# Kernel optimization log

Measured on AMD Instinct MI355X. Metric: run time of the kernel, lower is better.

Reference implementation:

```python
import jax, jax.numpy as jnp
import numpy as np

B, T, D = 2, 1024, 2048
H, HKV, DH = 16, 4, 128
G = H // HKV  # GQA groups
F = 5632
ROPE_THETA = 10000.0
EPS = 1e-6


def _rope_tables(t, dh, theta):
    inv = 1.0 / (theta ** (np.arange(0, dh, 2, dtype=np.float32) / dh))  # [dh//2]
    ang = np.outer(np.arange(t, dtype=np.float32), inv)                  # [T, dh//2]
    return jnp.asarray(np.cos(ang)), jnp.asarray(np.sin(ang))


def setup_inputs() -> dict:
    key = jax.random.key(0)
    ks = jax.random.split(key, 9)
    s = 0.02
    cos, sin = _rope_tables(T, DH, ROPE_THETA)
    return {
        "x": jax.random.normal(ks[0], (B, T, D), jnp.float32),
        "freqs_cos": cos,
        "freqs_sin": sin,
        "w_norm1": jnp.ones((D,), jnp.float32),
        "w_norm2": jnp.ones((D,), jnp.float32),
        "wq": jax.random.normal(ks[1], (D, H * DH), jnp.float32) * s,
        "wk": jax.random.normal(ks[2], (D, HKV * DH), jnp.float32) * s,
        "wv": jax.random.normal(ks[3], (D, HKV * DH), jnp.float32) * s,
        "wo": jax.random.normal(ks[4], (D, D), jnp.float32) * s,
        "w1": jax.random.normal(ks[5], (D, F), jnp.float32) * s,
        "w2": jax.random.normal(ks[6], (F, D), jnp.float32) * s,
        "w3": jax.random.normal(ks[7], (D, F), jnp.float32) * s,
    }


def _rmsnorm(x, w):
    var = jnp.mean(jnp.square(x), axis=-1, keepdims=True)
    return x * jax.lax.rsqrt(var + EPS) * w


def _apply_rope(x, cos, sin):
    # x: [B, T, nH, DH]; cos/sin: [T, DH//2]
    xr = x.reshape(*x.shape[:-1], DH // 2, 2)
    x0, x1 = xr[..., 0], xr[..., 1]
    c = cos[None, :, None, :]
    s = sin[None, :, None, :]
    o0 = x0 * c - x1 * s
    o1 = x0 * s + x1 * c
    return jnp.stack([o0, o1], axis=-1).reshape(x.shape)


def reference(x, freqs_cos, freqs_sin, w_norm1, w_norm2, wq, wk, wv, wo, w1, w2, w3):
    residual = x
    xn = _rmsnorm(x, w_norm1)
    q = (xn @ wq).reshape(B, T, H, DH)
    k = (xn @ wk).reshape(B, T, HKV, DH)
    v = (xn @ wv).reshape(B, T, HKV, DH)
    q = _apply_rope(q, freqs_cos, freqs_sin)
    k = _apply_rope(k, freqs_cos, freqs_sin)
    # grouped heads: q -> [B, HKV, G, T, DH]; k,v -> [B, HKV, T, DH]
    q = q.transpose(0, 2, 1, 3).reshape(B, HKV, G, T, DH)
    k = k.transpose(0, 2, 1, 3)
    v = v.transpose(0, 2, 1, 3)
    scale = DH ** -0.5
    scores = jnp.einsum("bkgtd,bksd->bkgts", q, k) * scale  # [B,HKV,G,T,T]
    causal = jnp.tril(jnp.ones((T, T), dtype=bool))
    scores = jnp.where(causal, scores, -jnp.inf)
    attn = jax.nn.softmax(scores, axis=-1)
    out = jnp.einsum("bkgts,bksd->bkgtd", attn, v)  # [B,HKV,G,T,DH]
    out = out.reshape(B, H, T, DH).transpose(0, 2, 1, 3).reshape(B, T, D)
    x = residual + out @ wo
    h = _rmsnorm(x, w_norm2)
    ffn = (jax.nn.silu(h @ w1) * (h @ w3)) @ w2
    return x + ffn
```

## Files before the change

### kernel.cpp

```cpp
#include <hip/hip_runtime.h>
#include <hip/hip_bf16.h>
#include <math.h>

typedef __hip_bfloat16 bf16;
typedef __attribute__((ext_vector_type(8))) short bf16x8;
typedef __attribute__((ext_vector_type(4))) float f32x4;

__device__ __forceinline__ float b2f(bf16 v) { return __bfloat162float(v); }
__device__ __forceinline__ bf16  f2b(float v) { return __float2bfloat16(v); }

constexpr int Bc = 2, Tc = 1024, Dc = 2048, Hc = 16, HKVc = 4, DHc = 128, Fc = 5632;
constexpr int Mr = Bc * Tc;
constexpr int Nqkv = Hc * DHc + 2 * HKVc * DHc;

__device__ __forceinline__ void g2l16(void* lds, const void* g) {
  __builtin_amdgcn_global_load_lds(
      (const __attribute__((address_space(1))) unsigned int*)g,
      (__attribute__((address_space(3))) unsigned int*)lds, 16, 0, 0);
}

__global__ __launch_bounds__(256) void tcast_k(const float* __restrict__ src,
                                               bf16* __restrict__ dst,
                                               int N, int K) {
  __shared__ bf16 tile[64][68];
  const int t = threadIdx.x;
  const int n0 = blockIdx.x * 64, k0 = blockIdx.y * 64;
#pragma unroll
  for (int it = 0; it < 4; ++it) {
    const int kl = it * 16 + (t >> 4);
    const int nl = (t & 15) * 4;
    float4 v = *reinterpret_cast<const float4*>(src + (size_t)(k0 + kl) * N + n0 + nl);
    tile[kl][nl]     = f2b(v.x);
    tile[kl][nl + 1] = f2b(v.y);
    tile[kl][nl + 2] = f2b(v.z);
    tile[kl][nl + 3] = f2b(v.w);
  }
  __syncthreads();
  union { uint4 u; bf16 h[8]; } o;
#pragma unroll
  for (int it = 0; it < 2; ++it) {
    const int nl = it * 32 + (t >> 3);
    const int kl = (t & 7) * 8;
#pragma unroll
    for (int j = 0; j < 8; ++j) o.h[j] = tile[kl + j][nl];
    *reinterpret_cast<uint4*>(dst + (size_t)(n0 + nl) * K + k0 + kl) = o.u;
  }
}

__global__ __launch_bounds__(256) void tcast_ffn(const float* __restrict__ src,
                                                 bf16* __restrict__ dst,
                                                 int off) {
  __shared__ bf16 tile[64][68];
  const int t = threadIdx.x;
  const int n0 = blockIdx.x * 64, k0 = blockIdx.y * 64;
#pragma unroll
  for (int it = 0; it < 4; ++it) {
    const int kl = it * 16 + (t >> 4);
    const int nl = (t & 15) * 4;
    float4 v = *reinterpret_cast<const float4*>(src + (size_t)(k0 + kl) * Fc + n0 + nl);
    tile[kl][nl]     = f2b(v.x);
    tile[kl][nl + 1] = f2b(v.y);
    tile[kl][nl + 2] = f2b(v.z);
    tile[kl][nl + 3] = f2b(v.w);
  }
  __syncthreads();
  union { uint4 u; bf16 h[8]; } o;
#pragma unroll
  for (int it = 0; it < 2; ++it) {
    const int nl = it * 32 + (t >> 3);
    const int kl = (t & 7) * 8;
#pragma unroll
    for (int j = 0; j < 8; ++j) o.h[j] = tile[kl + j][nl];
    const int n = n0 + nl;
    const int r = ((n >> 4) << 5) + (n & 15) + off;
    *reinterpret_cast<uint4*>(dst + (size_t)r * Dc + k0 + kl) = o.u;
  }
}

__global__ __launch_bounds__(256) void rmsnorm_k(const float* __restrict__ x,
                                                 const float* __restrict__ w,
                                                 bf16* __restrict__ out) {
  const size_t rbase = (size_t)blockIdx.x * Dc;
  float ss = 0.f;
  for (int i = threadIdx.x; i < Dc; i += 256) {
    float v = x[rbase + i];
    ss += v * v;
  }
#pragma unroll
  for (int off = 32; off > 0; off >>= 1) ss += __shfl_down(ss, off, 64);
  __shared__ float red[4];
  const int lane = threadIdx.x & 63, wid = threadIdx.x >> 6;
  if (lane == 0) red[wid] = ss;
  __syncthreads();
  const float scale = rsqrtf((red[0] + red[1] + red[2] + red[3]) / (float)Dc + 1e-6f);
  for (int i = threadIdx.x; i < Dc; i += 256)
    out[rbase + i] = f2b(x[rbase + i] * scale * w[i]);
}

__global__ __launch_bounds__(256) void reduce4_rms(const float* __restrict__ P,
                                                   const float* __restrict__ x,
                                                   const float* __restrict__ w,
                                                   float* __restrict__ xat,
                                                   bf16* __restrict__ hb) {
  constexpr size_t PS = (size_t)Mr * Dc;
  const size_t base4 = (size_t)blockIdx.x * (Dc / 4);
  const int t = threadIdx.x;
  float4 v[2];
  float ss = 0.f;
#pragma unroll
  for (int j = 0; j < 2; ++j) {
    const size_t c4 = base4 + t + j * 256;
    float4 a = reinterpret_cast<const float4*>(x)[c4];
#pragma unroll
    for (int z = 0; z < 4; ++z) {
      float4 q = reinterpret_cast<const float4*>(P + z * PS)[c4];
      a.x += q.x; a.y += q.y; a.z += q.z; a.w += q.w;
    }
    reinterpret_cast<float4*>(xat)[c4] = a;
    ss += a.x * a.x + a.y * a.y + a.z * a.z + a.w * a.w;
    v[j] = a;
  }
#pragma unroll
  for (int off = 32; off > 0; off >>= 1) ss += __shfl_down(ss, off, 64);
  __shared__ float red[4];
  const int lane = t & 63, wid = t >> 6;
  if (lane == 0) red[wid] = ss;
  __syncthreads();
  const float scale = rsqrtf((red[0] + red[1] + red[2] + red[3]) / (float)Dc + 1e-6f);
  bf16* hrow = hb + (size_t)blockIdx.x * Dc;
#pragma unroll
  for (int j = 0; j < 2; ++j) {
    const int c = (t + j * 256) * 4;
    hrow[c]     = f2b(v[j].x * scale * w[c]);
    hrow[c + 1] = f2b(v[j].y * scale * w[c + 1]);
    hrow[c + 2] = f2b(v[j].z * scale * w[c + 2]);
    hrow[c + 3] = f2b(v[j].w * scale * w[c + 3]);
  }
}

__global__ __launch_bounds__(256) void reduce4_add(const float* __restrict__ P,
                                                   const float* __restrict__ res,
                                                   float* __restrict__ out) {
  constexpr size_t PS = (size_t)Mr * Dc;
  const size_t c4 = (size_t)blockIdx.x * 256 + threadIdx.x;
  float4 a = reinterpret_cast<const float4*>(res)[c4];
#pragma unroll
  for (int z = 0; z < 4; ++z) {
    float4 q = reinterpret_cast<const float4*>(P + z * PS)[c4];
    a.x += q.x; a.y += q.y; a.z += q.z; a.w += q.w;
  }
  reinterpret_cast<float4*>(out)[c4] = a;
}

template <int K>
__global__ __launch_bounds__(512, 2) void ffn_gemm256(const bf16* __restrict__ A,
                                                      const bf16* __restrict__ B,
                                                      bf16* __restrict__ act) {
  constexpr int NT = K / 64;
  constexpr int NIT = NT / 2;
  __shared__ bf16 As[2 * 256 * 64];
  __shared__ bf16 Bs[3 * 256 * 64];
  const int tid = threadIdx.x;
  const int lane = tid & 63, wv = tid >> 6;
  const int wr = wv >> 2, wc = wv & 3;
  const int fr = lane & 15, quad = lane >> 4;
  const int swz = fr & 7;
  const int bm = blockIdx.y * 256;
  const int bn = blockIdx.x * 256;
  const int lrow = tid >> 3;
  const int scol = ((tid & 7) ^ (lrow & 7)) * 8;
  const size_t rstep = (size_t)64 * K;

  auto stageA = [&](int t, int half) {
    const int buf = (t & 1) * 16384;
    const bf16* g = A + (size_t)(bm + half * 128 + lrow) * K + t * 64 + scol;
    bf16* d = As + buf + half * 8192 + (size_t)tid * 8;
    g2l16(d, g);
    g2l16(d + 4096, g + rstep);
  };
  auto stageB = [&](int t, int half, int buf) {
    const bf16* g = B + (size_t)(bn + half * 128 + lrow) * K + t * 64 + scol;
    bf16* d = Bs + buf * 16384 + half * 8192 + (size_t)tid * 8;
    g2l16(d, g);
    g2l16(d + 4096, g + rstep);
  };

  f32x4 acc[8][4] = {};
  const int u0 = (quad ^ swz) * 8;

  stageA(0, 0); stageA(0, 1);
  stageB(0, 0, 0); stageB(0, 1, 0);
  stageB(1, 0, 1); stageB(1, 1, 1);
  asm volatile("s_waitcnt vmcnt(4)" ::: "memory");
  __builtin_amdgcn_s_barrier();

  int rb0 = 0, rb1 = 1, sb = 2;
  for (int it = 0; it < NIT; ++it) {
    const int t1 = 2 * it + 1;
#pragma unroll
    for (int j = 0; j < 8; ++j) {
      const int bufT = (j < 4) ? 0 : 16384;
      const int bufB = ((j < 4) ? rb0 : rb1) * 16384;
      const int qr4 = ((j & 3) >> 1) * 4, qc2 = ((j & 3) & 1) * 2;
      bf16x8 af[4][2], bv[2][2];
      const bf16* Ab = As + bufT + (size_t)(wr * 128 + fr) * 64;
      const bf16* Bb = Bs + bufB + (size_t)(wc * 64 + fr) * 64;
#pragma unroll
      for (int ii = 0; ii < 4; ++ii) {
        af[ii][0] = *reinterpret_cast<const bf16x8*>(Ab + (qr4 + ii) * 1024 + u0);
        af[ii][1] = *reinterpret_cast<const bf16x8*>(Ab + (qr4 + ii) * 1024 + (u0 ^ 32));
      }
#pragma unroll
      for (int jj = 0; jj < 2; ++jj) {
        bv[jj][0] = *reinterpret_cast<const bf16x8*>(Bb + (qc2 + jj) * 1024 + u0);
        bv[jj][1] = *reinterpret_cast<const bf16x8*>(Bb + (qc2 + jj) * 1024 + (u0 ^ 32));
      }
      if (j == 0)      stageA(t1, 0);
      else if (j == 1) stageA(t1, 1);
      else if (j == 2) { if (2 * it + 2 < NT) stageB(2 * it + 2, 0, sb); }
      else if (j == 3) { if (2 * it + 2 < NT) stageB(2 * it + 2, 1, sb); }
      else if (j == 4) { if (2 * it + 2 < NT) stageA(2 * it + 2, 0); }
      else if (j == 5) { if (2 * it + 2 < NT) stageA(2 * it + 2, 1); }
      else if (j == 6) { if (2 * it + 3 < NT) stageB(2 * it + 3, 0, rb0); }
      else             { if (2 * it + 3 < NT) stageB(2 * it + 3, 1, rb0); }
      __builtin_amdgcn_s_barrier();
      asm volatile("s_waitcnt lgkmcnt(0)" ::: "memory");
      __builtin_amdgcn_sched_barrier(0);
      __builtin_amdgcn_s_setprio(1);
#pragma unroll
      for (int ii = 0; ii < 4; ++ii)
#pragma unroll
        for (int jj = 0; jj < 2; ++jj) {
          acc[qr4 + ii][qc2 + jj] = __builtin_amdgcn_mfma_f32_16x16x32_bf16(
              af[ii][0], bv[jj][0], acc[qr4 + ii][qc2 + jj], 0, 0, 0);
          acc[qr4 + ii][qc2 + jj] = __builtin_amdgcn_mfma_f32_16x16x32_bf16(
              af[ii][1], bv[jj][1], acc[qr4 + ii][qc2 + jj], 0, 0, 0);
        }
      __builtin_amdgcn_s_setprio(0);
      if (j == 3) {
        if (2 * it + 2 < NT) asm volatile("s_waitcnt vmcnt(4)" ::: "memory");
        else                 asm volatile("s_waitcnt vmcnt(0)" ::: "memory");
      } else if (j == 7) {
        if (2 * it + 3 < NT)      asm volatile("s_waitcnt vmcnt(4)" ::: "memory");
        else if (2 * it + 2 < NT) asm volatile("s_waitcnt vmcnt(0)" ::: "memory");
      }
      __builtin_amdgcn_s_barrier();
    }
    const int nrb0 = sb; sb = rb1; rb1 = rb0; rb0 = nrb0;
  }

  const int er = quad * 4, ec = lane & 15;
#pragma unroll
  for (int i = 0; i < 8; ++i) {
    const int row = bm + wr * 128 + i * 16 + er;
#pragma unroll
    for (int jp = 0; jp < 2; ++jp) {
      const f32x4 g = acc[i][2 * jp], u = acc[i][2 * jp + 1];
      const int f = blockIdx.x * 128 + wc * 32 + jp * 16 + ec;
#pragma unroll
      for (int r = 0; r < 4; ++r) {
        const float sg = g[r] / (1.f + __expf(-g[r]));
        act[(size_t)(row + r) * Fc + f] = f2b(sg * u[r]);
      }
    }
  }
}

template <int KFULL, int KSUB>
__global__ __launch_bounds__(512, 2) void gemm256sk(const bf16* __restrict__ A,
                                                    const bf16* __restrict__ Bt,
                                                    float* __restrict__ Part,
                                                    int N) {
  constexpr int NT = KSUB / 64;
  constexpr int NIT = NT / 2;
  __shared__ bf16 As[2 * 256 * 64];
  __shared__ bf16 Bs[3 * 256 * 64];
  const int tid = threadIdx.x;
  const int lane = tid & 63, wv = tid >> 6;
  const int wr = wv >> 2, wc = wv & 3;
  const int fr = lane & 15, quad = lane >> 4;
  const int swz = fr & 7;
  const int bm = blockIdx.y * 256;
  const int bn = blockIdx.x * 256;
  const int kbase = blockIdx.z * KSUB;
  const int lrow = tid >> 3;
  const int scol = ((tid & 7) ^ (lrow & 7)) * 8;
  const size_t rstep = (size_t)64 * KFULL;

  auto stageA = [&](int t, int half) {
    const int buf = (t & 1) * 16384;
    const bf16* g = A + (size_t)(bm + half * 128 + lrow) * KFULL + kbase + t * 64 + scol;
    bf16* d = As + buf + half * 8192 + (size_t)tid * 8;
    g2l16(d, g);
    g2l16(d + 4096, g + rstep);
  };
  auto stageB = [&](int t, int half, int buf) {
    const bf16* g = Bt + (size_t)(bn + half * 128 + lrow) * KFULL + kbase + t * 64 + scol;
    bf16* d = Bs + buf * 16384 + half * 8192 + (size_t)tid * 8;
    g2l16(d, g);
    g2l16(d + 4096, g + rstep);
  };

  f32x4 acc[8][4] = {};
  const int u0 = (quad ^ swz) * 8;

  stageA(0, 0); stageA(0, 1);
  stageB(0, 0, 0); stageB(0, 1, 0);
  stageB(1, 0, 1); stageB(1, 1, 1);
  asm volatile("s_waitcnt vmcnt(4)" ::: "memory");
  __builtin_amdgcn_s_barrier();

  int rb0 = 0, rb1 = 1, sb = 2;
  for (int it = 0; it < NIT; ++it) {
    const int t1 = 2 * it + 1;
#pragma unroll
    for (int j = 0; j < 8; ++j) {
      const int bufT = (j < 4) ? 0 : 16384;
      const int bufB = ((j < 4) ? rb0 : rb1) * 16384;
      const int qr4 = ((j & 3) >> 1) * 4, qc2 = ((j & 3) & 1) * 2;
      bf16x8 af[4][2], bv[2][2];
      const bf16* Ab = As + bufT + (size_t)(wr * 128 + fr) * 64;
      const bf16* Bb = Bs + bufB + (size_t)(wc * 64 + fr) * 64;
#pragma unroll
      for (int ii = 0; ii < 4; ++ii) {
        af[ii][0] = *reinterpret_cast<const bf16x8*>(Ab + (qr4 + ii) * 1024 + u0);
        af[ii][1] = *reinterpret_cast<const bf16x8*>(Ab + (qr4 + ii) * 1024 + (u0 ^ 32));
      }
#pragma unroll
      for (int jj = 0; jj < 2; ++jj) {
        bv[jj][0] = *reinterpret_cast<const bf16x8*>(Bb + (qc2 + jj) * 1024 + u0);
        bv[jj][1] = *reinterpret_cast<const bf16x8*>(Bb + (qc2 + jj) * 1024 + (u0 ^ 32));
      }
      if (j == 0)      stageA(t1, 0);
      else if (j == 1) stageA(t1, 1);
      else if (j == 2) { if (2 * it + 2 < NT) stageB(2 * it + 2, 0, sb); }
      else if (j == 3) { if (2 * it + 2 < NT) stageB(2 * it + 2, 1, sb); }
      else if (j == 4) { if (2 * it + 2 < NT) stageA(2 * it + 2, 0); }
      else if (j == 5) { if (2 * it + 2 < NT) stageA(2 * it + 2, 1); }
      else if (j == 6) { if (2 * it + 3 < NT) stageB(2 * it + 3, 0, rb0); }
      else             { if (2 * it + 3 < NT) stageB(2 * it + 3, 1, rb0); }
      __builtin_amdgcn_s_barrier();
      asm volatile("s_waitcnt lgkmcnt(0)" ::: "memory");
      __builtin_amdgcn_sched_barrier(0);
      __builtin_amdgcn_s_setprio(1);
#pragma unroll
      for (int ii = 0; ii < 4; ++ii)
#pragma unroll
        for (int jj = 0; jj < 2; ++jj) {
          acc[qr4 + ii][qc2 + jj] = __builtin_amdgcn_mfma_f32_16x16x32_bf16(
              af[ii][0], bv[jj][0], acc[qr4 + ii][qc2 + jj], 0, 0, 0);
          acc[qr4 + ii][qc2 + jj] = __builtin_amdgcn_mfma_f32_16x16x32_bf16(
              af[ii][1], bv[jj][1], acc[qr4 + ii][qc2 + jj], 0, 0, 0);
        }
      __builtin_amdgcn_s_setprio(0);
      if (j == 3) {
        if (2 * it + 2 < NT) asm volatile("s_waitcnt vmcnt(4)" ::: "memory");
        else                 asm volatile("s_waitcnt vmcnt(0)" ::: "memory");
      } else if (j == 7) {
        if (2 * it + 3 < NT)      asm volatile("s_waitcnt vmcnt(4)" ::: "memory");
        else if (2 * it + 2 < NT) asm volatile("s_waitcnt vmcnt(0)" ::: "memory");
      }
      __builtin_amdgcn_s_barrier();
    }
    const int nrb0 = sb; sb = rb1; rb1 = rb0; rb0 = nrb0;
  }

  float* P = Part + (size_t)blockIdx.z * ((size_t)Mr * N);
  const int er = quad * 4, ec = lane & 15;
#pragma unroll
  for (int i = 0; i < 8; ++i) {
    const int row = bm + wr * 128 + i * 16 + er;
#pragma unroll
    for (int jc = 0; jc < 4; ++jc) {
      const int col = bn + wc * 64 + jc * 16 + ec;
#pragma unroll
      for (int r = 0; r < 4; ++r)
        P[(size_t)(row + r) * N + col] = acc[i][jc][r];
    }
  }
}

__global__ __launch_bounds__(256) void repack_k(const float* __restrict__ P,
                                                const float* __restrict__ cosb,
                                                const float* __restrict__ sinb,
                                                bf16* __restrict__ Qr,
                                                bf16* __restrict__ Kr,
                                                bf16* __restrict__ Vt) {
  constexpr size_t PS = (size_t)Mr * Nqkv;
  const int bt = blockIdx.x;
  const int b = bt >> 10, tp = bt & (Tc - 1);
  const int t0 = threadIdx.x;
  const float* r0 = P + (size_t)bt * Nqkv;
  const float* r1 = r0 + PS;
#pragma unroll
  for (int k = 0; k < 4; ++k) {
    int p2 = k * 256 + t0;
    int hh = p2 >> 6, i = p2 & 63;
    float c = cosb[tp * 64 + i], sn = sinb[tp * 64 + i];
    float2 v0 = *reinterpret_cast<const float2*>(r0 + hh * 128 + 2 * i);
    float2 v1 = *reinterpret_cast<const float2*>(r1 + hh * 128 + 2 * i);
    float x0 = v0.x + v1.x, x1 = v0.y + v1.y;
    bf16* dst = Qr + ((size_t)(b * Hc + hh) * Tc + tp) * DHc + 2 * i;
    dst[0] = f2b(x0 * c - x1 * sn);
    dst[1] = f2b(x0 * sn + x1 * c);
  }
  {
    int hh = t0 >> 6, i = t0 & 63;
    float c = cosb[tp * 64 + i], sn = sinb[tp * 64 + i];
    float2 v0 = *reinterpret_cast<const float2*>(r0 + 2048 + hh * 128 + 2 * i);
    float2 v1 = *reinterpret_cast<const float2*>(r1 + 2048 + hh * 128 + 2 * i);
    float x0 = v0.x + v1.x, x1 = v0.y + v1.y;
    bf16* dst = Kr + ((size_t)(b * HKVc + hh) * Tc + tp) * DHc + 2 * i;
    dst[0] = f2b(x0 * c - x1 * sn);
    dst[1] = f2b(x0 * sn + x1 * c);
  }
#pragma unroll
  for (int k = 0; k < 2; ++k) {
    int e = k * 256 + t0;
    int kvh = e >> 7, dd = e & 127;
    Vt[((size_t)(b * HKVc + kvh) * DHc + dd) * Tc + tp] = f2b(r0[2560 + e] + r1[2560 + e]);
  }
}

__global__ __launch_bounds__(256) void fattn(const bf16* __restrict__ Qr,
                                             const bf16* __restrict__ Kr,
                                             const bf16* __restrict__ Vt,
                                             bf16* __restrict__ ao) {
  __shared__ __align__(16) bf16 Ks[2][64 * 128];
  __shared__ __align__(16) bf16 Vts[2][128 * 64];
  __shared__ __align__(16) bf16 Ps[4][16 * 72];
  const int idx = blockIdx.x;
  const int r = idx & 15;
  const int qt = (r & 1) ? (15 - (r >> 1)) : (r >> 1);
  const int h = (idx >> 4) & 15;
  const int b = idx >> 8;
  const int kv = h >> 2;
  const int t = threadIdx.x, lane = t & 63, wv = t >> 6;
  const int fr = lane & 15, quad = lane >> 4;

  const bf16* Qbase = Qr + ((size_t)(b * Hc + h) * Tc + qt * 64) * DHc;
  const bf16* Kbase = Kr + (size_t)(b * HKVc + kv) * Tc * DHc;
  const bf16* Vbase = Vt + (size_t)(b * HKVc + kv) * DHc * Tc;

  auto stageK = [&](int kt, int buf) {
    const bf16* src = Kbase + (size_t)kt * 64 * DHc;
#pragma unroll
    for (int rr = 0; rr < 4; ++rr) {
      const int row = rr * 16 + (t >> 4);
      const int cS = (t & 15) ^ (row & 7);
      g2l16(&Ks[buf][rr * 2048 + t * 8], src + row * DHc + cS * 8);
    }
  };
  auto stageV = [&](int kt, int buf) {
#pragma unroll
    for (int rr = 0; rr < 4; ++rr) {
      const int row = rr * 32 + (t >> 3);
      const int cS = (t & 7) ^ (row & 7);
      g2l16(&Vts[buf][rr * 2048 + t * 8], Vbase + (size_t)row * Tc + kt * 64 + cS * 8);
    }
  };

  bf16x8 qf[4];
#pragma unroll
  for (int c = 0; c < 4; ++c)
    qf[c] = *reinterpret_cast<const bf16x8*>(Qbase + (size_t)(wv * 16 + fr) * DHc + c * 32 + quad * 8);

  float m[4], l[4];
  f32x4 o[8] = {};
#pragma unroll
  for (int r2 = 0; r2 < 4; ++r2) { m[r2] = -3.0e38f; l[r2] = 0.f; }

  stageK(0, 0);
  stageV(0, 0);
  __syncthreads();
  int buf = 0;

  for (int kt = 0; kt <= qt; ++kt) {
    if (kt < qt) { stageK(kt + 1, buf ^ 1); stageV(kt + 1, buf ^ 1); }
    const int sw = fr & 7;
    f32x4 s[4];
    __builtin_amdgcn_s_setprio(1);
#pragma unroll
    for (int cb = 0; cb < 4; ++cb) {
      f32x4 acc = {};
#pragma unroll
      for (int kc = 0; kc < 4; ++kc) {
        bf16x8 kf = *reinterpret_cast<const bf16x8*>(
            &Ks[buf][(cb * 16 + fr) * 128 + (((kc << 2) + quad) ^ sw) * 8]);
        acc = __builtin_amdgcn_mfma_f32_16x16x32_bf16(qf[kc], kf, acc, 0, 0, 0);
      }
      s[cb] = acc * 0.08838834764831845f;
    }
    __builtin_amdgcn_s_setprio(0);
    if (kt == qt) {
#pragma unroll
      for (int cb = 0; cb < 4; ++cb)
#pragma unroll
        for (int r2 = 0; r2 < 4; ++r2) {
          int key = cb * 16 + fr;
          int qg = wv * 16 + quad * 4 + r2;
          if (key > qg) s[cb][r2] = -3.0e38f;
        }
    }
    float tm[4], ts[4];
#pragma unroll
    for (int r2 = 0; r2 < 4; ++r2)
      tm[r2] = fmaxf(fmaxf(s[0][r2], s[1][r2]), fmaxf(s[2][r2], s[3][r2]));
#pragma unroll
    for (int off = 1; off < 16; off <<= 1)
#pragma unroll
      for (int r2 = 0; r2 < 4; ++r2)
        tm[r2] = fmaxf(tm[r2], __shfl_xor(tm[r2], off, 64));
    float al[4];
#pragma unroll
    for (int r2 = 0; r2 < 4; ++r2) {
      float mn = fmaxf(m[r2], tm[r2]);
      al[r2] = __expf(m[r2] - mn);
      m[r2] = mn;
      ts[r2] = 0.f;
    }
#pragma unroll
    for (int cb = 0; cb < 4; ++cb)
#pragma unroll
      for (int r2 = 0; r2 < 4; ++r2) {
        float e = __expf(s[cb][r2] - m[r2]);
        s[cb][r2] = e;
        ts[r2] += e;
      }
#pragma unroll
    for (int off = 1; off < 16; off <<= 1)
#pragma unroll
      for (int r2 = 0; r2 < 4; ++r2)
        ts[r2] += __shfl_xor(ts[r2], off, 64);
#pragma unroll
    for (int r2 = 0; r2 < 4; ++r2) l[r2] = l[r2] * al[r2] + ts[r2];
#pragma unroll
    for (int db = 0; db < 8; ++db)
#pragma unroll
      for (int r2 = 0; r2 < 4; ++r2) o[db][r2] *= al[r2];
    bf16* pw = Ps[wv];
#pragma unroll
    for (int cb = 0; cb < 4; ++cb)
#pragma unroll
      for (int r2 = 0; r2 < 4; ++r2)
        pw[(quad * 4 + r2) * 72 + cb * 16 + fr] = f2b(s[cb][r2]);
    bf16x8 pa[2];
    pa[0] = *reinterpret_cast<const bf16x8*>(&pw[fr * 72 + quad * 8]);
    pa[1] = *reinterpret_cast<const bf16x8*>(&pw[fr * 72 + 32 + quad * 8]);
    __builtin_amdgcn_s_setprio(1);
#pragma unroll
    for (int db = 0; db < 8; ++db) {
      bf16x8 v0 = *reinterpret_cast<const bf16x8*>(
          &Vts[buf][(db * 16 + fr) * 64 + (quad ^ sw) * 8]);
      bf16x8 v1 = *reinterpret_cast<const bf16x8*>(
          &Vts[buf][(db * 16 + fr) * 64 + ((4 + quad) ^ sw) * 8]);
      o[db] = __builtin_amdgcn_mfma_f32_16x16x32_bf16(pa[0], v0, o[db], 0, 0, 0);
      o[db] = __builtin_amdgcn_mfma_f32_16x16x32_bf16(pa[1], v1, o[db], 0, 0, 0);
    }
    __builtin_amdgcn_s_setprio(0);
    __syncthreads();
    buf ^= 1;
  }
#pragma unroll
  for (int r2 = 0; r2 < 4; ++r2) {
    float inv = 1.f / l[r2];
    int qg = qt * 64 + wv * 16 + quad * 4 + r2;
    bf16* orow = ao + (size_t)(b * Tc + qg) * Dc + h * DHc;
#pragma unroll
    for (int db = 0; db < 8; ++db)
      orow[db * 16 + fr] = f2b(o[db][r2] * inv);
  }
}

extern "C" void kernel_launch(void* const* d_in, const int* in_sizes, int n_in,
                              void* d_out, int out_size, void* d_ws, size_t ws_size,
                              hipStream_t stream) {
  const float* x    = (const float*)d_in[0];
  const float* fcos = (const float*)d_in[1];
  const float* fsin = (const float*)d_in[2];
  const float* wn1  = (const float*)d_in[3];
  const float* wn2  = (const float*)d_in[4];
  const float* wq   = (const float*)d_in[5];
  const float* wk   = (const float*)d_in[6];
  const float* wv   = (const float*)d_in[7];
  const float* wo   = (const float*)d_in[8];
  const float* w1   = (const float*)d_in[9];
  const float* w2   = (const float*)d_in[10];
  const float* w3   = (const float*)d_in[11];

  char* p = (char*)d_ws;
  bf16* wqkv_t = (bf16*)p;                 p += (size_t)Nqkv * Dc * 2;
  float* xat   = (float*)d_ws;
  bf16* wo_t = (bf16*)p;                   p += (size_t)Dc * Dc * 2;
  bf16* w13t = (bf16*)p;                   p += (size_t)2 * Fc * Dc * 2;
  bf16* w2t  = w13t;
  bf16* xn   = (bf16*)p;                   p += (size_t)Mr * Dc * 2;
  bf16* ao   = (bf16*)p;                   p += (size_t)Mr * Dc * 2;
  bf16* act  = (bf16*)p;                   p += (size_t)Mr * Fc * 2;
  float* Pbuf = (float*)p;                 p += (size_t)4 * Mr * Dc * 4;
  bf16* hb = xn;
  bf16* Qr = act;
  bf16* Kr = act + (size_t)Mr * Hc * DHc;
  bf16* Vtb = Kr + (size_t)Mr * HKVc * DHc;

  const dim3 blk(256);
  tcast_k<<<dim3(32, 32), blk, 0, stream>>>(wq, wqkv_t, 2048, 2048);
  tcast_k<<<dim3(8, 32), blk, 0, stream>>>(wk, wqkv_t + (size_t)2048 * 2048, 512, 2048);
  tcast_k<<<dim3(8, 32), blk, 0, stream>>>(wv, wqkv_t + (size_t)2560 * 2048, 512, 2048);
  tcast_k<<<dim3(32, 32), blk, 0, stream>>>(wo, wo_t, 2048, 2048);
  tcast_ffn<<<dim3(88, 32), blk, 0, stream>>>(w1, w13t, 0);
  tcast_ffn<<<dim3(88, 32), blk, 0, stream>>>(w3, w13t, 16);

  rmsnorm_k<<<Mr, blk, 0, stream>>>(x, wn1, xn);
  gemm256sk<Dc, 1024><<<dim3(Nqkv / 256, Mr / 256, 2), dim3(512), 0, stream>>>(xn, wqkv_t, Pbuf, Nqkv);
  repack_k<<<Mr, blk, 0, stream>>>(Pbuf, fcos, fsin, Qr, Kr, Vtb);
  fattn<<<Bc * Hc * 16, blk, 0, stream>>>(Qr, Kr, Vtb, ao);
  gemm256sk<Dc, 512><<<dim3(Dc / 256, Mr / 256, 4), dim3(512), 0, stream>>>(ao, wo_t, Pbuf, Dc);
  reduce4_rms<<<Mr, blk, 0, stream>>>(Pbuf, x, wn2, xat, hb);
  ffn_gemm256<Dc><<<dim3(2 * Fc / 256, Mr / 256), dim3(512), 0, stream>>>(hb, w13t, act);
  tcast_k<<<dim3(32, 88), blk, 0, stream>>>(w2, w2t, 2048, 5632);
  gemm256sk<Fc, 1408><<<dim3(Dc / 256, Mr / 256, 4), dim3(512), 0, stream>>>(act, w2t, Pbuf, Dc);
  reduce4_add<<<Mr * Dc / 1024, blk, 0, stream>>>(Pbuf, xat, (float*)d_out);
}
```

Measured before the change: 561.0 us.

## Fuse weight transposes into GEMM launches to overlap casts with compute

Merges the wq/wk/wv transpose-casts and the first rmsnorm into one launch. It also folds the wo/w1/w3 transpose-casts into the QKV GEMM grid and the w2 transpose-cast into the FFN gate/up GEMM grid, with extra blocks taking the bandwidth-bound cast work. The goal is to cut launch count and let memory-bound casting run alongside MFMA-bound GEMM tiles. The w2 cast gets its own workspace region when space allows, so it no longer has to wait for the w13 buffer to be freed. The cost is larger monolithic kernels with 160KB of LDS per block for the cast blocks, which may limit occupancy for the cast work.

Measured after the change: 529.7 us. 1.06x faster.

```diff
diff --git a/kernel.cpp b/kernel.cpp
--- a/kernel.cpp
+++ b/kernel.cpp
@@ -19,12 +19,10 @@
       (__attribute__((address_space(3))) unsigned int*)lds, 16, 0, 0);
 }
 
-__global__ __launch_bounds__(256) void tcast_k(const float* __restrict__ src,
-                                               bf16* __restrict__ dst,
-                                               int N, int K) {
-  __shared__ bf16 tile[64][68];
-  const int t = threadIdx.x;
-  const int n0 = blockIdx.x * 64, k0 = blockIdx.y * 64;
+__device__ __forceinline__ void tcast_tile(const float* __restrict__ src,
+                                           bf16* __restrict__ dst,
+                                           int N, int K, int n0, int k0,
+                                           int t, bf16 (*tile)[68]) {
 #pragma unroll
   for (int it = 0; it < 4; ++it) {
     const int kl = it * 16 + (t >> 4);
@@ -47,12 +45,10 @@
   }
 }
 
-__global__ __launch_bounds__(256) void tcast_ffn(const float* __restrict__ src,
-                                                 bf16* __restrict__ dst,
-                                                 int off) {
-  __shared__ bf16 tile[64][68];
-  const int t = threadIdx.x;
-  const int n0 = blockIdx.x * 64, k0 = blockIdx.y * 64;
+__device__ __forceinline__ void tcast_ffn_tile(const float* __restrict__ src,
+                                               bf16* __restrict__ dst, int off,
+                                               int n0, int k0, int t,
+                                               bf16 (*tile)[68]) {
 #pragma unroll
   for (int it = 0; it < 4; ++it) {
     const int kl = it * 16 + (t >> 4);
@@ -77,10 +73,11 @@
   }
 }
 
-__global__ __launch_bounds__(256) void rmsnorm_k(const float* __restrict__ x,
-                                                 const float* __restrict__ w,
-                                                 bf16* __restrict__ out) {
-  const size_t rbase = (size_t)blockIdx.x * Dc;
+__device__ __forceinline__ void rmsnorm_row(const float* __restrict__ x,
+                                            const float* __restrict__ w,
+                                            bf16* __restrict__ out,
+                                            int row, float* red) {
+  const size_t rbase = (size_t)row * Dc;
   float ss = 0.f;
   for (int i = threadIdx.x; i < Dc; i += 256) {
     float v = x[rbase + i];
@@ -88,13 +85,34 @@
   }
 #pragma unroll
   for (int off = 32; off > 0; off >>= 1) ss += __shfl_down(ss, off, 64);
-  __shared__ float red[4];
   const int lane = threadIdx.x & 63, wid = threadIdx.x >> 6;
   if (lane == 0) red[wid] = ss;
   __syncthreads();
   const float scale = rsqrtf((red[0] + red[1] + red[2] + red[3]) / (float)Dc + 1e-6f);
   for (int i = threadIdx.x; i < Dc; i += 256)
     out[rbase + i] = f2b(x[rbase + i] * scale * w[i]);
+}
+
+__global__ __launch_bounds__(256) void prep1(const float* __restrict__ wq,
+                                             const float* __restrict__ wk,
+                                             const float* __restrict__ wv,
+                                             const float* __restrict__ x,
+                                             const float* __restrict__ wn1,
+                                             bf16* __restrict__ wqkv_t,
+                                             bf16* __restrict__ xn) {
+  __shared__ __align__(16) bf16 tile[64][68];
+  const int b = blockIdx.x;
+  if (b < 1024) {
+    tcast_tile(wq, wqkv_t, 2048, 2048, (b & 31) * 64, (b >> 5) * 64, threadIdx.x, tile);
+  } else if (b < 1280) {
+    const int r = b - 1024;
+    tcast_tile(wk, wqkv_t + (size_t)2048 * 2048, 512, 2048, (r & 7) * 64, (r >> 3) * 64, threadIdx.x, tile);
+  } else if (b < 1536) {
+    const int r = b - 1280;
+    tcast_tile(wv, wqkv_t + (size_t)2560 * 2048, 512, 2048, (r & 7) * 64, (r >> 3) * 64, threadIdx.x, tile);
+  } else {
+    rmsnorm_row(x, wn1, xn, b - 1536, (float*)tile);
+  }
 }
 
 __global__ __launch_bounds__(256) void reduce4_rms(const float* __restrict__ P,
@@ -152,21 +170,174 @@
   reinterpret_cast<float4*>(out)[c4] = a;
 }
 
-template <int K>
-__global__ __launch_bounds__(512, 2) void ffn_gemm256(const bf16* __restrict__ A,
-                                                      const bf16* __restrict__ B,
-                                                      bf16* __restrict__ act) {
-  constexpr int NT = K / 64;
+template <int KFULL, int KSUB>
+__device__ __forceinline__ void gemm256sk_dev(const bf16* __restrict__ A,
+                                              const bf16* __restrict__ Bt,
+                                              float* __restrict__ Part,
+                                              int N, int bx, int by, int bz,
+                                              char* smem) {
+  constexpr int NT = KSUB / 64;
   constexpr int NIT = NT / 2;
-  __shared__ bf16 As[2 * 256 * 64];
-  __shared__ bf16 Bs[3 * 256 * 64];
+  bf16* As = (bf16*)smem;
+  bf16* Bs = (bf16*)(smem + 65536);
   const int tid = threadIdx.x;
   const int lane = tid & 63, wv = tid >> 6;
   const int wr = wv >> 2, wc = wv & 3;
   const int fr = lane & 15, quad = lane >> 4;
   const int swz = fr & 7;
-  const int bm = blockIdx.y * 256;
-  const int bn = blockIdx.x * 256;
+  const int bm = by * 256;
+  const int bn = bx * 256;
+  const int kbase = bz * KSUB;
+  const int lrow = tid >> 3;
+  const int scol = ((tid & 7) ^ (lrow & 7)) * 8;
+  const size_t rstep = (size_t)64 * KFULL;
+
+  auto stageA = [&](int t, int half) {
+    const int buf = (t & 1) * 16384;
+    const bf16* g = A + (size_t)(bm + half * 128 + lrow) * KFULL + kbase + t * 64 + scol;
+    bf16* d = As + buf + half * 8192 + (size_t)tid * 8;
+    g2l16(d, g);
+    g2l16(d + 4096, g + rstep);
+  };
+  auto stageB = [&](int t, int half, int buf) {
+    const bf16* g = Bt + (size_t)(bn + half * 128 + lrow) * KFULL + kbase + t * 64 + scol;
+    bf16* d = Bs + buf * 16384 + half * 8192 + (size_t)tid * 8;
+    g2l16(d, g);
+    g2l16(d + 4096, g + rstep);
+  };
+
+  f32x4 acc[8][4] = {};
+  const int u0 = (quad ^ swz) * 8;
+
+  stageA(0, 0); stageA(0, 1);
+  stageB(0, 0, 0); stageB(0, 1, 0);
+  stageB(1, 0, 1); stageB(1, 1, 1);
+  asm volatile("s_waitcnt vmcnt(4)" ::: "memory");
+  __builtin_amdgcn_s_barrier();
+
+  int rb0 = 0, rb1 = 1, sb = 2;
+  for (int it = 0; it < NIT; ++it) {
+    const int t1 = 2 * it + 1;
+#pragma unroll
+    for (int j = 0; j < 8; ++j) {
+      const int bufT = (j < 4) ? 0 : 16384;
+      const int bufB = ((j < 4) ? rb0 : rb1) * 16384;
+      const int qr4 = ((j & 3) >> 1) * 4, qc2 = ((j & 3) & 1) * 2;
+      bf16x8 af[4][2], bv[2][2];
+      const bf16* Ab = As + bufT + (size_t)(wr * 128 + fr) * 64;
+      const bf16* Bb = Bs + bufB + (size_t)(wc * 64 + fr) * 64;
+#pragma unroll
+      for (int ii = 0; ii < 4; ++ii) {
+        af[ii][0] = *reinterpret_cast<const bf16x8*>(Ab + (qr4 + ii) * 1024 + u0);
+        af[ii][1] = *reinterpret_cast<const bf16x8*>(Ab + (qr4 + ii) * 1024 + (u0 ^ 32));
+      }
+#pragma unroll
+      for (int jj = 0; jj < 2; ++jj) {
+        bv[jj][0] = *reinterpret_cast<const bf16x8*>(Bb + (qc2 + jj) * 1024 + u0);
+        bv[jj][1] = *reinterpret_cast<const bf16x8*>(Bb + (qc2 + jj) * 1024 + (u0 ^ 32));
+      }
+      if (j == 0)      stageA(t1, 0);
+      else if (j == 1) stageA(t1, 1);
+      else if (j == 2) { if (2 * it + 2 < NT) stageB(2 * it + 2, 0, sb); }
+      else if (j == 3) { if (2 * it + 2 < NT) stageB(2 * it + 2, 1, sb); }
+      else if (j == 4) { if (2 * it + 2 < NT) stageA(2 * it + 2, 0); }
+      else if (j == 5) { if (2 * it + 2 < NT) stageA(2 * it + 2, 1); }
+      else if (j == 6) { if (2 * it + 3 < NT) stageB(2 * it + 3, 0, rb0); }
+      else             { if (2 * it + 3 < NT) stageB(2 * it + 3, 1, rb0); }
+      __builtin_amdgcn_s_barrier();
+      asm volatile("s_waitcnt lgkmcnt(0)" ::: "memory");
+      __builtin_amdgcn_sched_barrier(0);
+      __builtin_amdgcn_s_setprio(1);
+#pragma unroll
+      for (int ii = 0; ii < 4; ++ii)
+#pragma unroll
+        for (int jj = 0; jj < 2; ++jj) {
+          acc[qr4 + ii][qc2 + jj] = __builtin_amdgcn_mfma_f32_16x16x32_bf16(
+              af[ii][0], bv[jj][0], acc[qr4 + ii][qc2 + jj], 0, 0, 0);
+          acc[qr4 + ii][qc2 + jj] = __builtin_amdgcn_mfma_f32_16x16x32_bf16(
+              af[ii][1], bv[jj][1], acc[qr4 + ii][qc2 + jj], 0, 0, 0);
+        }
+      __builtin_amdgcn_s_setprio(0);
+      if (j == 3) {
+        if (2 * it + 2 < NT) asm volatile("s_waitcnt vmcnt(4)" ::: "memory");
+        else                 asm volatile("s_waitcnt vmcnt(0)" ::: "memory");
+      } else if (j == 7) {
+        if (2 * it + 3 < NT)      asm volatile("s_waitcnt vmcnt(4)" ::: "memory");
+        else if (2 * it + 2 < NT) asm volatile("s_waitcnt vmcnt(0)" ::: "memory");
+      }
+      __builtin_amdgcn_s_barrier();
+    }
+    const int nrb0 = sb; sb = rb1; rb1 = rb0; rb0 = nrb0;
+  }
+
+  float* P = Part + (size_t)bz * ((size_t)Mr * N);
+  const int er = quad * 4, ec = lane & 15;
+#pragma unroll
+  for (int i = 0; i < 8; ++i) {
+    const int row = bm + wr * 128 + i * 16 + er;
+#pragma unroll
+    for (int jc = 0; jc < 4; ++jc) {
+      const int col = bn + wc * 64 + jc * 16 + ec;
+#pragma unroll
+      for (int r = 0; r < 4; ++r)
+        P[(size_t)(row + r) * N + col] = acc[i][jc][r];
+    }
+  }
+}
+
+template <int KFULL, int KSUB>
+__global__ __launch_bounds__(512, 2) void gemm256sk(const bf16* __restrict__ A,
+                                                    const bf16* __restrict__ Bt,
+                                                    float* __restrict__ Part,
+                                                    int N) {
+  __shared__ __align__(16) char smem[163840];
+  gemm256sk_dev<KFULL, KSUB>(A, Bt, Part, N, blockIdx.x, blockIdx.y, blockIdx.z, smem);
+}
+
+__global__ __launch_bounds__(512, 2) void qkv_mega(const bf16* __restrict__ A,
+                                                   const bf16* __restrict__ Bt,
+                                                   float* __restrict__ Part,
+                                                   const float* __restrict__ wo,
+                                                   bf16* __restrict__ wo_t,
+                                                   const float* __restrict__ w1,
+                                                   const float* __restrict__ w3,
+                                                   bf16* __restrict__ w13t) {
+  __shared__ __align__(16) char smem[163840];
+  const int b = blockIdx.x;
+  if (b < 192) {
+    gemm256sk_dev<Dc, 1024>(A, Bt, Part, Nqkv, b % 12, (b / 12) % 8, b / 96, smem);
+  } else {
+    const int sub = threadIdx.x >> 8, t = threadIdx.x & 255;
+    bf16 (*tile)[68] = reinterpret_cast<bf16(*)[68]>(smem + sub * 8704);
+    if (b < 704) {
+      const int tt = (b - 192) * 2 + sub;
+      tcast_tile(wo, wo_t, 2048, 2048, (tt & 31) * 64, (tt >> 5) * 64, t, tile);
+    } else if (b < 2112) {
+      const int tt = (b - 704) * 2 + sub;
+      tcast_ffn_tile(w1, w13t, 0, (tt % 88) * 64, (tt / 88) * 64, t, tile);
+    } else {
+      const int tt = (b - 2112) * 2 + sub;
+      tcast_ffn_tile(w3, w13t, 16, (tt % 88) * 64, (tt / 88) * 64, t, tile);
+    }
+  }
+}
+
+template <int K>
+__device__ __forceinline__ void ffn_dev(const bf16* __restrict__ A,
+                                        const bf16* __restrict__ B,
+                                        bf16* __restrict__ act,
+                                        int bx, int by, char* smem) {
+  constexpr int NT = K / 64;
+  constexpr int NIT = NT / 2;
+  bf16* As = (bf16*)smem;
+  bf16* Bs = (bf16*)(smem + 65536);
+  const int tid = threadIdx.x;
+  const int lane = tid & 63, wv = tid >> 6;
+  const int wr = wv >> 2, wc = wv & 3;
+  const int fr = lane & 15, quad = lane >> 4;
+  const int swz = fr & 7;
+  const int bm = by * 256;
+  const int bn = bx * 256;
   const int lrow = tid >> 3;
   const int scol = ((tid & 7) ^ (lrow & 7)) * 8;
   const size_t rstep = (size_t)64 * K;
@@ -256,7 +427,7 @@
 #pragma unroll
     for (int jp = 0; jp < 2; ++jp) {
       const f32x4 g = acc[i][2 * jp], u = acc[i][2 * jp + 1];
-      const int f = blockIdx.x * 128 + wc * 32 + jp * 16 + ec;
+      const int f = bx * 128 + wc * 32 + jp * 16 + ec;
 #pragma unroll
       for (int r = 0; r < 4; ++r) {
         const float sg = g[r] / (1.f + __expf(-g[r]));
@@ -266,118 +437,28 @@
   }
 }
 
-template <int KFULL, int KSUB>
-__global__ __launch_bounds__(512, 2) void gemm256sk(const bf16* __restrict__ A,
-                                                    const bf16* __restrict__ Bt,
-                                                    float* __restrict__ Part,
-                                                    int N) {
-  constexpr int NT = KSUB / 64;
-  constexpr int NIT = NT / 2;
-  __shared__ bf16 As[2 * 256 * 64];
-  __shared__ bf16 Bs[3 * 256 * 64];
-  const int tid = threadIdx.x;
-  const int lane = tid & 63, wv = tid >> 6;
-  const int wr = wv >> 2, wc = wv & 3;
-  const int fr = lane & 15, quad = lane >> 4;
-  const int swz = fr & 7;
-  const int bm = blockIdx.y * 256;
-  const int bn = blockIdx.x * 256;
-  const int kbase = blockIdx.z * KSUB;
-  const int lrow = tid >> 3;
-  const int scol = ((tid & 7) ^ (lrow & 7)) * 8;
-  const size_t rstep = (size_t)64 * KFULL;
-
-  auto stageA = [&](int t, int half) {
-    const int buf = (t & 1) * 16384;
-    const bf16* g = A + (size_t)(bm + half * 128 + lrow) * KFULL + kbase + t * 64 + scol;
-    bf16* d = As + buf + half * 8192 + (size_t)tid * 8;
-    g2l16(d, g);
-    g2l16(d + 4096, g + rstep);
-  };
-  auto stageB = [&](int t, int half, int buf) {
-    const bf16* g = Bt + (size_t)(bn + half * 128 + lrow) * KFULL + kbase + t * 64 + scol;
-    bf16* d = Bs + buf * 16384 + half * 8192 + (size_t)tid * 8;
-    g2l16(d, g);
-    g2l16(d + 4096, g + rstep);
-  };
-
-  f32x4 acc[8][4] = {};
-  const int u0 = (quad ^ swz) * 8;
-
-  stageA(0, 0); stageA(0, 1);
-  stageB(0, 0, 0); stageB(0, 1, 0);
-  stageB(1, 0, 1); stageB(1, 1, 1);
-  asm volatile("s_waitcnt vmcnt(4)" ::: "memory");
-  __builtin_amdgcn_s_barrier();
-
-  int rb0 = 0, rb1 = 1, sb = 2;
-  for (int it = 0; it < NIT; ++it) {
-    const int t1 = 2 * it + 1;
-#pragma unroll
-    for (int j = 0; j < 8; ++j) {
-      const int bufT = (j < 4) ? 0 : 16384;
-      const int bufB = ((j < 4) ? rb0 : rb1) * 16384;
-      const int qr4 = ((j & 3) >> 1) * 4, qc2 = ((j & 3) & 1) * 2;
-      bf16x8 af[4][2], bv[2][2];
-      const bf16* Ab = As + bufT + (size_t)(wr * 128 + fr) * 64;
-      const bf16* Bb = Bs + bufB + (size_t)(wc * 64 + fr) * 64;
-#pragma unroll
-      for (int ii = 0; ii < 4; ++ii) {
-        af[ii][0] = *reinterpret_cast<const bf16x8*>(Ab + (qr4 + ii) * 1024 + u0);
-        af[ii][1] = *reinterpret_cast<const bf16x8*>(Ab + (qr4 + ii) * 1024 + (u0 ^ 32));
-      }
-#pragma unroll
-      for (int jj = 0; jj < 2; ++jj) {
-        bv[jj][0] = *reinterpret_cast<const bf16x8*>(Bb + (qc2 + jj) * 1024 + u0);
-        bv[jj][1] = *reinterpret_cast<const bf16x8*>(Bb + (qc2 + jj) * 1024 + (u0 ^ 32));
-      }
-      if (j == 0)      stageA(t1, 0);
-      else if (j == 1) stageA(t1, 1);
-      else if (j == 2) { if (2 * it + 2 < NT) stageB(2 * it + 2, 0, sb); }
-      else if (j == 3) { if (2 * it + 2 < NT) stageB(2 * it + 2, 1, sb); }
-      else if (j == 4) { if (2 * it + 2 < NT) stageA(2 * it + 2, 0); }
-      else if (j == 5) { if (2 * it + 2 < NT) stageA(2 * it + 2, 1); }
-      else if (j == 6) { if (2 * it + 3 < NT) stageB(2 * it + 3, 0, rb0); }
-      else             { if (2 * it + 3 < NT) stageB(2 * it + 3, 1, rb0); }
-      __builtin_amdgcn_s_barrier();
-      asm volatile("s_waitcnt lgkmcnt(0)" ::: "memory");
-      __builtin_amdgcn_sched_barrier(0);
-      __builtin_amdgcn_s_setprio(1);
-#pragma unroll
-      for (int ii = 0; ii < 4; ++ii)
-#pragma unroll
-        for (int jj = 0; jj < 2; ++jj) {
-          acc[qr4 + ii][qc2 + jj] = __builtin_amdgcn_mfma_f32_16x16x32_bf16(
-              af[ii][0], bv[jj][0], acc[qr4 + ii][qc2 + jj], 0, 0, 0);
-          acc[qr4 + ii][qc2 + jj] = __builtin_amdgcn_mfma_f32_16x16x32_bf16(
-              af[ii][1], bv[jj][1], acc[qr4 + ii][qc2 + jj], 0, 0, 0);
-        }
-      __builtin_amdgcn_s_setprio(0);
-      if (j == 3) {
-        if (2 * it + 2 < NT) asm volatile("s_waitcnt vmcnt(4)" ::: "memory");
-        else                 asm volatile("s_waitcnt vmcnt(0)" ::: "memory");
-      } else if (j == 7) {
-        if (2 * it + 3 < NT)      asm volatile("s_waitcnt vmcnt(4)" ::: "memory");
-        else if (2 * it + 2 < NT) asm volatile("s_waitcnt vmcnt(0)" ::: "memory");
-      }
-      __builtin_amdgcn_s_barrier();
-    }
-    const int nrb0 = sb; sb = rb1; rb1 = rb0; rb0 = nrb0;
-  }
-
-  float* P = Part + (size_t)blockIdx.z * ((size_t)Mr * N);
-  const int er = quad * 4, ec = lane & 15;
-#pragma unroll
-  for (int i = 0; i < 8; ++i) {
-    const int row = bm + wr * 128 + i * 16 + er;
-#pragma unroll
-    for (int jc = 0; jc < 4; ++jc) {
-      const int col = bn + wc * 64 + jc * 16 + ec;
-#pragma unroll
-      for (int r = 0; r < 4; ++r)
-        P[(size_t)(row + r) * N + col] = acc[i][jc][r];
-    }
-  }
+__global__ __launch_bounds__(512, 2) void ffn_mega(const bf16* __restrict__ A,
+                                                   const bf16* __restrict__ B,
+                                                   bf16* __restrict__ act,
+                                                   const float* __restrict__ w2,
+                                                   bf16* __restrict__ w2t) {
+  __shared__ __align__(16) char smem[163840];
+  const int b = blockIdx.x;
+  if (b < 352) {
+    ffn_dev<Dc>(A, B, act, b % 44, b / 44, smem);
+  } else {
+    const int sub = threadIdx.x >> 8, t = threadIdx.x & 255;
+    bf16 (*tile)[68] = reinterpret_cast<bf16(*)[68]>(smem + sub * 8704);
+    const int tt = (b - 352) * 2 + sub;
+    tcast_tile(w2, w2t, 2048, 5632, (tt & 31) * 64, (tt >> 5) * 64, t, tile);
+  }
+}
+
+__global__ __launch_bounds__(256) void tcast_k(const float* __restrict__ src,
+                                               bf16* __restrict__ dst,
+                                               int N, int K) {
+  __shared__ __align__(16) bf16 tile[64][68];
+  tcast_tile(src, dst, N, K, blockIdx.x * 64, blockIdx.y * 64, threadIdx.x, tile);
 }
 
 __global__ __launch_bounds__(256) void repack_k(const float* __restrict__ P,
@@ -593,7 +674,6 @@
   float* xat   = (float*)d_ws;
   bf16* wo_t = (bf16*)p;                   p += (size_t)Dc * Dc * 2;
   bf16* w13t = (bf16*)p;                   p += (size_t)2 * Fc * Dc * 2;
-  bf16* w2t  = w13t;
   bf16* xn   = (bf16*)p;                   p += (size_t)Mr * Dc * 2;
   bf16* ao   = (bf16*)p;                   p += (size_t)Mr * Dc * 2;
   bf16* act  = (bf16*)p;                   p += (size_t)Mr * Fc * 2;
@@ -602,23 +682,24 @@
   bf16* Qr = act;
   bf16* Kr = act + (size_t)Mr * Hc * DHc;
   bf16* Vtb = Kr + (size_t)Mr * HKVc * DHc;
+  const size_t w2t_bytes = (size_t)Dc * Fc * 2;
+  const size_t base_used = (size_t)(p - (char*)d_ws);
+  const bool fused_w2 = (ws_size >= base_used + w2t_bytes);
+  bf16* w2t = fused_w2 ? (bf16*)p : w13t;
 
   const dim3 blk(256);
-  tcast_k<<<dim3(32, 32), blk, 0, stream>>>(wq, wqkv_t, 2048, 2048);
-  tcast_k<<<dim3(8, 32), blk, 0, stream>>>(wk, wqkv_t + (size_t)2048 * 2048, 512, 2048);
-  tcast_k<<<dim3(8, 32), blk, 0, stream>>>(wv, wqkv_t + (size_t)2560 * 2048, 512, 2048);
-  tcast_k<<<dim3(32, 32), blk, 0, stream>>>(wo, wo_t, 2048, 2048);
-  tcast_ffn<<<dim3(88, 32), blk, 0, stream>>>(w1, w13t, 0);
-  tcast_ffn<<<dim3(88, 32), blk, 0, stream>>>(w3, w13t, 16);
-
-  rmsnorm_k<<<Mr, blk, 0, stream>>>(x, wn1, xn);
-  gemm256sk<Dc, 1024><<<dim3(Nqkv / 256, Mr / 256, 2), dim3(512), 0, stream>>>(xn, wqkv_t, Pbuf, Nqkv);
+  prep1<<<3584, blk, 0, stream>>>(wq, wk, wv, x, wn1, wqkv_t, xn);
+  qkv_mega<<<3520, dim3(512), 0, stream>>>(xn, wqkv_t, Pbuf, wo, wo_t, w1, w3, w13t);
   repack_k<<<Mr, blk, 0, stream>>>(Pbuf, fcos, fsin, Qr, Kr, Vtb);
   fattn<<<Bc * Hc * 16, blk, 0, stream>>>(Qr, Kr, Vtb, ao);
   gemm256sk<Dc, 512><<<dim3(Dc / 256, Mr / 256, 4), dim3(512), 0, stream>>>(ao, wo_t, Pbuf, Dc);
   reduce4_rms<<<Mr, blk, 0, stream>>>(Pbuf, x, wn2, xat, hb);
-  ffn_gemm256<Dc><<<dim3(2 * Fc / 256, Mr / 256), dim3(512), 0, stream>>>(hb, w13t, act);
-  tcast_k<<<dim3(32, 88), blk, 0, stream>>>(w2, w2t, 2048, 5632);
+  if (fused_w2) {
+    ffn_mega<<<352 + 1408, dim3(512), 0, stream>>>(hb, w13t, act, w2, w2t);
+  } else {
+    ffn_mega<<<352, dim3(512), 0, stream>>>(hb, w13t, act, w2, w2t);
+    tcast_k<<<dim3(32, 88), blk, 0, stream>>>(w2, w2t, 2048, 5632);
+  }
   gemm256sk<Fc, 1408><<<dim3(Dc / 256, Mr / 256, 4), dim3(512), 0, stream>>>(act, w2t, Pbuf, Dc);
   reduce4_add<<<Mr * Dc / 1024, blk, 0, stream>>>(Pbuf, xat, (float*)d_out);
 }
```
